# Optimization experiments

Hardware: AMD Instinct MI355X
Metric: run time of the kernel (lower is better)

Reference implementation:

```python
import jax, jax.numpy as jnp
import numpy as np

B, S, H = 16, 128, 768
L, K = 2, 4
NORM_ITEM = 0.5


def _xavier(key, shape):
    fan_in, fan_out = shape[-1], shape[-2]
    std = float(np.sqrt(2.0 / (fan_in + fan_out)))
    return jax.random.normal(key, shape, dtype=jnp.float32) * std


def setup_inputs() -> dict:
    key = jax.random.key(0)
    ks = jax.random.split(key, 13)
    sentences = jax.random.normal(ks[0], (B, S, H), dtype=jnp.float32)
    adj_matrix = jax.random.uniform(ks[1], (B, K, S, S), dtype=jnp.float32)
    return {
        "sentences": sentences,
        "adj_matrix": adj_matrix,
        # stacked per-(layer, dep_kind) parameters
        "W_in": _xavier(ks[2], (L, K, H, H)),
        "b_in": _xavier(ks[3], (L, K, H, 1)),
        "W_out": _xavier(ks[4], (L, K, H, H)),
        "b_out": _xavier(ks[5], (L, K, H, 1)),
        "Wg_in": _xavier(ks[6], (L, K, H, H)),
        "bg_in": _xavier(ks[7], (L, K, H, 1)),
        "Wg_out": _xavier(ks[8], (L, K, H, H)),
        "bg_out": _xavier(ks[9], (L, K, H, 1)),
        "W_loop": _xavier(ks[10], (L, H, H)),
    }


def reference(sentences, adj_matrix, W_in, b_in, W_out, b_out,
              Wg_in, bg_in, Wg_out, bg_out, W_loop):
    # sentences: [B,S,H], adj_matrix: [B,K,S,S]
    adj_in = adj_matrix                       # message along edges
    adj_out = jnp.swapaxes(adj_matrix, 2, 3)  # reversed edges
    h = jnp.swapaxes(sentences, 1, 2)         # [B,H,S]

    def conv(Wg, bg, W, b, adj, h):
        # Wg,W: [K,H,H]; bg,b: [K,H,1]; adj: [B,K,S,S]; h: [B,H,S]
        gate = jax.nn.sigmoid(jnp.einsum('khd,bds->bkhs', Wg, h) + bg[None])
        rel = NORM_ITEM * gate * (jnp.einsum('khd,bds->bkhs', W, h) + b[None])
        # bmm with adjacency, then sum over dep kinds
        return jnp.einsum('bkhs,bkst->bht', rel, adj)

    n_layers = W_in.shape[0]
    for l in range(n_layers):
        s = jnp.einsum('hd,bds->bhs', W_loop[l], h)  # self loop
        s = s + conv(Wg_in[l], bg_in[l], W_in[l], b_in[l], adj_in, h)
        s = s + conv(Wg_out[l], bg_out[l], W_out[l], b_out[l], adj_out, h)
        h = jax.nn.relu(s)
    return jnp.swapaxes(h, 1, 2)  # [B,S,H]
```

## Files before the change

kernel.cpp:

```cpp
#include <hip/hip_runtime.h>
#include <stdint.h>

#define B_ 16
#define S_ 128
#define H_ 768
#define K_ 4
#define L_ 2
#define T_ (B_*S_)

typedef __attribute__((ext_vector_type(4))) float f32x4;
typedef __attribute__((ext_vector_type(8))) short s16x8;
typedef __bf16 bf16x8 __attribute__((ext_vector_type(8)));
typedef unsigned short u16;

__device__ inline u16 f2bf(float f) {
    union { float f; uint32_t u; } v; v.f = f;
    uint32_t u = v.u;
    return (u16)((u + 0x7fffu + ((u >> 16) & 1u)) >> 16);
}

__device__ inline ushort4 f2bf4(float4 v) {
    ushort4 r; r.x = f2bf(v.x); r.y = f2bf(v.y); r.z = f2bf(v.z); r.w = f2bf(v.w);
    return r;
}

template <typename T>
__device__ inline auto mfma_impl(T a, T b, f32x4 c, int)
    -> decltype(__builtin_amdgcn_mfma_f32_16x16x32_bf16(a, b, c, 0, 0, 0)) {
    return __builtin_amdgcn_mfma_f32_16x16x32_bf16(a, b, c, 0, 0, 0);
}
template <typename T>
__device__ inline f32x4 mfma_impl(T a, T b, f32x4 c, long) {
    return __builtin_amdgcn_mfma_f32_16x16x32_bf16(
        __builtin_bit_cast(bf16x8, a), __builtin_bit_cast(bf16x8, b), c, 0, 0, 0);
}
__device__ inline f32x4 mfma16(s16x8 a, s16x8 b, f32x4 c) {
    return mfma_impl(a, b, c, 0);
}

__device__ inline void gload_lds16(const void* g, void* l) {
    __builtin_amdgcn_global_load_lds(
        (__attribute__((address_space(1))) void*)(g),
        (__attribute__((address_space(3))) void*)(l), 16, 0, 0);
}

__device__ inline void stage_tile(const char* gbase, int rowStrideBytes, u16* lds, int tid) {
    const int lane = tid & 63;
    const int w = tid >> 6;
    const int lr = lane >> 3;
    const int cb = (lane & 7) << 4;
    #pragma unroll
    for (int j = 0; j < 4; ++j) {
        const int seg = j * 4 + w;
        const int row = seg * 8 + lr;
        const int sb = cb ^ ((row & 7) << 4);
        gload_lds16(gbase + (size_t)row * rowStrideBytes + sb, lds + seg * 512);
    }
}

__device__ inline void stage64(const char* gbase, int rowStrideBytes, char* lds, int tid) {
    const int lane = tid & 63;
    const int w = tid >> 6;
    const int lr = lane >> 3;
    const int cb = (lane & 7) << 4;
    #pragma unroll
    for (int j = 0; j < 2; ++j) {
        const int seg = j * 4 + w;
        const int row = seg * 8 + lr;
        const int sb = cb ^ ((row & 7) << 4);
        gload_lds16(gbase + (size_t)row * rowStrideBytes + sb, lds + seg * 1024);
    }
}

__device__ inline s16x8 read_frag(const u16* lds, int row, int colByte) {
    const int bir = colByte ^ ((row & 7) << 4);
    return *(const s16x8*)((const char*)lds + row * 128 + bir);
}

__device__ inline s16x8 rf32s(const u16* lds, int row, int cb) {
    const int bir = cb ^ (((row >> 1) & 3) << 4);
    return *(const s16x8*)((const char*)lds + row * 64 + bir);
}

__global__ void prep_x(const float* __restrict__ sent, u16* __restrict__ X0) {
    const int i4 = blockIdx.x * blockDim.x + threadIdx.x;
    if (i4 < T_ * H_ / 4) ((ushort4*)X0)[i4] = f2bf4(((const float4*)sent)[i4]);
}

__global__ void prep_adj(const float* __restrict__ adj, u16* __restrict__ adjA) {
    const int idx = blockIdx.x * blockDim.x + threadIdx.x;
    const int s = idx & 127;
    const int t = (idx >> 7) & 127;
    const int b = (idx >> 14) & 15;
    const int p = idx >> 18;
    const int dir = p >> 2, k = p & 3;
    const float v = dir ? adj[(((size_t)b * K_ + k) * S_ + t) * S_ + s]
                        : adj[(((size_t)b * K_ + k) * S_ + s) * S_ + t];
    adjA[idx] = f2bf(v);
}

__global__ void pack_weights(const float* __restrict__ W_in,  const float* __restrict__ W_out,
                             const float* __restrict__ Wg_in, const float* __restrict__ Wg_out,
                             const float* __restrict__ W_loop, u16* __restrict__ Wpk) {
    __shared__ float slab[16][772];
    const int tid = threadIdx.x;
    const int bid = blockIdx.x;
    const int nT  = bid % 48;
    const int mat = (bid / 48) % 17;
    const int l   = bid / (48 * 17);

    const float* src;
    if (mat < 16) {
        const int p = mat >> 1, slot = mat & 1;
        const int dir = p >> 2, k = p & 3;
        const float* t = slot ? (dir ? Wg_out : Wg_in) : (dir ? W_out : W_in);
        src = t + ((size_t)l * K_ + k) * (H_ * H_);
    } else {
        src = W_loop + (size_t)l * (H_ * H_);
    }
    #pragma unroll
    for (int it = 0; it < 12; ++it) {
        const int idx = it * 256 + tid;
        const int row = idx / 192, c4 = idx % 192;
        *(float4*)&slab[row][c4 * 4] = ((const float4*)(src + (size_t)(nT * 16 + row) * H_))[c4];
    }
    __syncthreads();
    const int q = tid >> 6, lane = tid & 63;
    const int n = lane & 15, ks = lane >> 4;
    u16* outBase = Wpk + ((((size_t)l * 17 + mat) * 48 + nT) * 24) * 512;
    #pragma unroll
    for (int it = 0; it < 6; ++it) {
        const int kT = it * 4 + q;
        u16 tmp[8];
        #pragma unroll
        for (int u = 0; u < 8; ++u) tmp[u] = f2bf(slab[n][kT * 32 + ks * 8 + u]);
        s16x8 v;
        #pragma unroll
        for (int u = 0; u < 8; ++u) v[u] = (short)tmp[u];
        *(s16x8*)(outBase + (size_t)kT * 512 + lane * 8) = v;
    }
}

__global__ __launch_bounds__(256, 2)
void gemm1_kernel(const u16* __restrict__ Xb, const u16* __restrict__ Wpk,
                  const float* __restrict__ bg_in, const float* __restrict__ bg_out,
                  const float* __restrict__ b_in,  const float* __restrict__ b_out,
                  int layer,
                  u16* __restrict__ Rel2, float* __restrict__ SBuf) {
    __shared__ __align__(16) char smem[16384];

    const int tid = threadIdx.x;
    const int lane = tid & 63;
    const int w = tid >> 6;
    const int wm = w >> 1;
    const int wn = w & 1;
    const int l15 = lane & 15;
    const int hi16 = (lane >> 4) << 4;

    const int id = blockIdx.x;
    const int id2 = (id & 7) * 102 + (id >> 3);
    int p, y, m;
    if (id2 < 768) { p = id2 / 96; const int r = id2 % 96; y = r / 16; m = r % 16; }
    else           { const int q = id2 - 768; p = 8; y = q / 16; m = q % 16; }
    const int m0 = m * 128;

    const u16* pkL = Wpk + (size_t)layer * 17 * 589824;
    const int matR = (p < 8) ? p * 2     : 16;
    const int matG = (p < 8) ? p * 2 + 1 : 16;
    const int nbr  = (p < 8) ? y * 8     : y * 16;
    const int nbg  = (p < 8) ? y * 8     : y * 16 + 8;
    const u16* pR = pkL + ((size_t)matR * 48 + nbr + wn * 4) * (24 * 512) + lane * 8;
    const u16* pG = pkL + ((size_t)matG * 48 + nbg + wn * 4) * (24 * 512) + lane * 8;
    const char* gA = (const char*)Xb + (size_t)m0 * (H_ * 2);

    auto STAGE_A = [&](int kt, int c) {
        char* base = smem + c * 8192;
        #pragma unroll
        for (int j = 0; j < 2; ++j) {
            const int rr = (j * 4 + w) * 16 + (lane >> 2);
            const int cbl = (lane & 3) << 4;
            const int sc = cbl ^ (((rr >> 1) & 3) << 4);
            gload_lds16(gA + (size_t)rr * (H_ * 2) + kt * 64 + sc,
                        base + (j * 4 + w) * 1024);
        }
    };
    auto LOADB = [&](s16x8* dst, int kt) {
        #pragma unroll
        for (int j = 0; j < 4; ++j) {
            dst[j]     = *(const s16x8*)(pR + ((size_t)j * 24 + kt) * 512);
            dst[4 + j] = *(const s16x8*)(pG + ((size_t)j * 24 + kt) * 512);
        }
    };

    const f32x4 zf = {0.f, 0.f, 0.f, 0.f};
    f32x4 accr[4][4], accg[4][4];
    #pragma unroll
    for (int i = 0; i < 4; ++i)
        #pragma unroll
        for (int j = 0; j < 4; ++j) { accr[i][j] = zf; accg[i][j] = zf; }

    s16x8 bA[8], bB[8];

    STAGE_A(0, 0);
    __builtin_amdgcn_sched_barrier(0);
    LOADB(bA, 0);

    auto body = [&](int t, s16x8* cur, s16x8* nxt, bool pf) {
        asm volatile("s_waitcnt vmcnt(8)" ::: "memory");
        __builtin_amdgcn_s_barrier();
        const u16* lA = (const u16*)(smem + (t & 1) * 8192);
        s16x8 a[4];
        #pragma unroll
        for (int i = 0; i < 4; ++i)
            a[i] = rf32s(lA, wm * 64 + i * 16 + l15, hi16);
        if (pf) {
            STAGE_A(t + 1, (t + 1) & 1);
            __builtin_amdgcn_sched_barrier(0);
            LOADB(nxt, t + 1);
        }
        __builtin_amdgcn_s_setprio(1);
        #pragma unroll
        for (int i = 0; i < 4; ++i) {
            #pragma unroll
            for (int j = 0; j < 4; ++j) {
                accr[i][j] = mfma16(a[i], cur[j],     accr[i][j]);
                accg[i][j] = mfma16(a[i], cur[4 + j], accg[i][j]);
            }
        }
        __builtin_amdgcn_s_setprio(0);
    };

    for (int t = 0; t < 24; t += 2) {
        body(t,     bA, bB, true);
        body(t + 1, bB, bA, t + 1 < 23);
    }

    if (p < 8) {
        const int dir = p >> 2, k = p & 3;
        const float* bgp = (dir ? bg_out : bg_in) + ((size_t)layer * K_ + k) * H_;
        const float* brp = (dir ? b_out  : b_in ) + ((size_t)layer * K_ + k) * H_;
        #pragma unroll
        for (int j = 0; j < 4; ++j) {
            const int h = y * 128 + wn * 64 + j * 16 + l15;
            const float bgv = bgp[h];
            const float brv = brp[h];
            #pragma unroll
            for (int i = 0; i < 4; ++i) {
                const int s0 = wm * 64 + i * 16 + ((lane >> 4) << 2);
                u16 tmp[4];
                #pragma unroll
                for (int r = 0; r < 4; ++r) {
                    const float g = accg[i][j][r] + bgv;
                    const float v = accr[i][j][r] + brv;
                    tmp[r] = f2bf(0.5f * v / (1.f + __expf(-g)));
                }
                ushort4 pk; pk.x = tmp[0]; pk.y = tmp[1]; pk.z = tmp[2]; pk.w = tmp[3];
                *(ushort4*)(Rel2 + (((size_t)p * B_ + m) * H_ + h) * S_ + s0) = pk;
            }
        }
    } else {
        #pragma unroll
        for (int j = 0; j < 4; ++j) {
            const int h1 = y * 256 + wn * 64 + j * 16 + l15;
            const int h2 = h1 + 128;
            #pragma unroll
            for (int i = 0; i < 4; ++i) {
                const int tg = m0 + wm * 64 + i * 16 + ((lane >> 4) << 2);
                #pragma unroll
                for (int r = 0; r < 4; ++r) {
                    SBuf[(size_t)(tg + r) * H_ + h1] = accr[i][j][r];
                    SBuf[(size_t)(tg + r) * H_ + h2] = accg[i][j][r];
                }
            }
        }
    }
}

__global__ __launch_bounds__(256, 2)
void gemm2_kernel(const u16* __restrict__ adjA, const u16* __restrict__ Rel2,
                  const float* __restrict__ SBuf,
                  u16* __restrict__ Xn, float* __restrict__ Out, int lastLayer) {
    __shared__ __align__(16) char smem2[49152];

    const int tid = threadIdx.x;
    const int lane = tid & 63;
    const int w = tid >> 6;
    const int wm = w >> 1, wn = w & 1;
    const int l15 = lane & 15;
    const int hi16 = (lane >> 4) << 4;
    const int h0 = blockIdx.x * 64;
    const int b = blockIdx.y;

    auto STAGE = [&](int q, int c) {
        const int p = q >> 1, sc = q & 1;
        const char* Ab = (const char*)adjA + ((size_t)p * B_ + b) * (S_ * S_ * 2) + sc * 128;
        const char* Bb = (const char*)Rel2 + (((size_t)p * B_ + b) * H_ + h0) * (S_ * 2) + sc * 128;
        char* base = smem2 + c * 24576;
        stage_tile(Ab, S_ * 2, (u16*)base, tid);
        stage64(Bb, S_ * 2, base + 16384, tid);
    };

    const f32x4 zf = {0.f, 0.f, 0.f, 0.f};
    f32x4 acc[4][2];
    #pragma unroll
    for (int i = 0; i < 4; ++i)
        #pragma unroll
        for (int j = 0; j < 2; ++j) acc[i][j] = zf;

    STAGE(0, 0);
    __syncthreads();

    for (int q = 0; q < 16; ++q) {
        const int c = q & 1;
        if (q < 15) STAGE(q + 1, c ^ 1);
        const u16* lA = (const u16*)(smem2 + c * 24576);
        const u16* lB = (const u16*)(smem2 + c * 24576 + 16384);
        #pragma unroll
        for (int kq = 0; kq < 2; ++kq) {
            const int ck = kq * 64 + hi16;
            s16x8 a[4], bb[2];
            #pragma unroll
            for (int i = 0; i < 4; ++i)
                a[i] = read_frag(lA, wm * 64 + i * 16 + l15, ck);
            #pragma unroll
            for (int j = 0; j < 2; ++j)
                bb[j] = read_frag(lB, wn * 32 + j * 16 + l15, ck);
            #pragma unroll
            for (int i = 0; i < 4; ++i)
                #pragma unroll
                for (int j = 0; j < 2; ++j)
                    acc[i][j] = mfma16(a[i], bb[j], acc[i][j]);
        }
        __syncthreads();
    }

    #pragma unroll
    for (int i = 0; i < 4; ++i) {
        const int tl = wm * 64 + i * 16 + ((lane >> 4) << 2);
        #pragma unroll
        for (int j = 0; j < 2; ++j) {
            const int h = h0 + wn * 32 + j * 16 + l15;
            #pragma unroll
            for (int r = 0; r < 4; ++r) {
                const size_t t = (size_t)b * S_ + tl + r;
                float v = acc[i][j][r] + SBuf[t * H_ + h];
                v = fmaxf(v, 0.f);
                if (lastLayer) Out[t * H_ + h] = v;
                else           Xn[t * H_ + h] = f2bf(v);
            }
        }
    }
}

extern "C" void kernel_launch(void* const* d_in, const int* in_sizes, int n_in,
                              void* d_out, int out_size, void* d_ws, size_t ws_size,
                              hipStream_t stream) {
    const float* sent   = (const float*)d_in[0];
    const float* adj    = (const float*)d_in[1];
    const float* W_in   = (const float*)d_in[2];
    const float* b_in   = (const float*)d_in[3];
    const float* W_out  = (const float*)d_in[4];
    const float* b_out  = (const float*)d_in[5];
    const float* Wg_in  = (const float*)d_in[6];
    const float* bg_in  = (const float*)d_in[7];
    const float* Wg_out = (const float*)d_in[8];
    const float* bg_out = (const float*)d_in[9];
    const float* W_loop = (const float*)d_in[10];

    char* ws = (char*)d_ws;
    u16* Wpk    = (u16*)(ws);
    u16* adjA   = (u16*)(ws + 40108032);
    u16* X0     = (u16*)(ws + 44302336);
    u16* X1     = (u16*)(ws + 47448064);
    u16* Rel2   = (u16*)(ws + 50593792);
    float* SBuf = (float*)(ws + 75759616);

    prep_x<<<1536, 256, 0, stream>>>(sent, X0);
    prep_adj<<<8192, 256, 0, stream>>>(adj, adjA);
    pack_weights<<<L_ * 17 * 48, 256, 0, stream>>>(W_in, W_out, Wg_in, Wg_out, W_loop, Wpk);

    u16* Xc = X0;
    u16* Xn = X1;
    for (int l = 0; l < L_; ++l) {
        gemm1_kernel<<<816, 256, 0, stream>>>(Xc, Wpk, bg_in, bg_out, b_in, b_out,
                                              l, Rel2, SBuf);
        gemm2_kernel<<<dim3(12, 16), 256, 0, stream>>>(adjA, Rel2, SBuf, Xn,
                                                       (float*)d_out, l == L_ - 1);
        u16* t = Xc; Xc = Xn; Xn = t;
    }
}
```

Measured before the change: 186.6 us.

## Stage A tiles in 128-wide K chunks with 64KB LDS double buffer in gemm1

gemm1 now stages the activation tile into LDS in K-chunks of 128 (four MFMA sub-steps) instead of 32, using a 64KB double buffer with a new XOR swizzle. This cuts the number of block barriers from 24 to 6. B-fragment register loads are interleaved between the sub-steps. The cost is much higher LDS use per block, which may limit occupancy to about two blocks per CU.

```diff
diff --git a/kernel.cpp b/kernel.cpp
--- a/kernel.cpp
+++ b/kernel.cpp
@@ -77,9 +77,9 @@
     return *(const s16x8*)((const char*)lds + row * 128 + bir);
 }
 
-__device__ inline s16x8 rf32s(const u16* lds, int row, int cb) {
-    const int bir = cb ^ (((row >> 1) & 3) << 4);
-    return *(const s16x8*)((const char*)lds + row * 64 + bir);
+__device__ inline s16x8 rfA(const u16* lds, int row, int cb) {
+    const int bir = cb ^ ((row & 7) << 4);
+    return *(const s16x8*)((const char*)lds + row * 256 + bir);
 }
 
 __global__ void prep_x(const float* __restrict__ sent, u16* __restrict__ X0) {
@@ -147,7 +147,7 @@
                   const float* __restrict__ b_in,  const float* __restrict__ b_out,
                   int layer,
                   u16* __restrict__ Rel2, float* __restrict__ SBuf) {
-    __shared__ __align__(16) char smem[16384];
+    __shared__ __align__(16) char smem[65536];
 
     const int tid = threadIdx.x;
     const int lane = tid & 63;
@@ -155,7 +155,8 @@
     const int wm = w >> 1;
     const int wn = w & 1;
     const int l15 = lane & 15;
-    const int hi16 = (lane >> 4) << 4;
+    const int ks = lane >> 4;
+    const int hi16 = ks << 4;
 
     const int id = blockIdx.x;
     const int id2 = (id & 7) * 102 + (id >> 3);
@@ -173,15 +174,14 @@
     const u16* pG = pkL + ((size_t)matG * 48 + nbg + wn * 4) * (24 * 512) + lane * 8;
     const char* gA = (const char*)Xb + (size_t)m0 * (H_ * 2);
 
-    auto STAGE_A = [&](int kt, int c) {
-        char* base = smem + c * 8192;
-        #pragma unroll
-        for (int j = 0; j < 2; ++j) {
-            const int rr = (j * 4 + w) * 16 + (lane >> 2);
-            const int cbl = (lane & 3) << 4;
-            const int sc = cbl ^ (((rr >> 1) & 3) << 4);
-            gload_lds16(gA + (size_t)rr * (H_ * 2) + kt * 64 + sc,
-                        base + (j * 4 + w) * 1024);
+    auto STAGE_A = [&](int S, int c) {
+        char* base = smem + c * 32768;
+        #pragma unroll
+        for (int j = 0; j < 8; ++j) {
+            const int row = j * 16 + w * 4 + ks;
+            const int sc = (l15 << 4) ^ ((row & 7) << 4);
+            gload_lds16(gA + (size_t)row * (H_ * 2) + S * 256 + sc,
+                        base + j * 4096 + w * 1024);
         }
     };
     auto LOADB = [&](s16x8* dst, int kt) {
@@ -201,39 +201,44 @@
 
     s16x8 bA[8], bB[8];
 
+    #define DO_SUB(LA, KTL, BUF)                                               \
+        {                                                                      \
+            s16x8 a[4];                                                        \
+            _Pragma("unroll") for (int i = 0; i < 4; ++i)                      \
+                a[i] = rfA(LA, wm * 64 + i * 16 + l15, (KTL) * 64 + hi16);     \
+            __builtin_amdgcn_s_setprio(1);                                     \
+            _Pragma("unroll") for (int i = 0; i < 4; ++i) {                    \
+                _Pragma("unroll") for (int j = 0; j < 4; ++j) {                \
+                    accr[i][j] = mfma16(a[i], BUF[j],     accr[i][j]);         \
+                    accg[i][j] = mfma16(a[i], BUF[4 + j], accg[i][j]);         \
+                }                                                              \
+            }                                                                  \
+            __builtin_amdgcn_s_setprio(0);                                     \
+        }
+
     STAGE_A(0, 0);
+    LOADB(bA, 0);
+    asm volatile("s_waitcnt vmcnt(0)" ::: "memory");
+    __builtin_amdgcn_s_barrier();
     __builtin_amdgcn_sched_barrier(0);
-    LOADB(bA, 0);
-
-    auto body = [&](int t, s16x8* cur, s16x8* nxt, bool pf) {
+
+    for (int S = 0; S < 6; ++S) {
+        const u16* lA = (const u16*)(smem + (S & 1) * 32768);
+        const int k0 = S * 4;
+        LOADB(bB, k0 + 1);
+        if (S < 5) STAGE_A(S + 1, (S & 1) ^ 1);
+        DO_SUB(lA, 0, bA)
+        LOADB(bA, k0 + 2);
+        DO_SUB(lA, 1, bB)
+        LOADB(bB, k0 + 3);
+        DO_SUB(lA, 2, bA)
+        if (S < 5) LOADB(bA, k0 + 4);
+        DO_SUB(lA, 3, bB)
         asm volatile("s_waitcnt vmcnt(8)" ::: "memory");
         __builtin_amdgcn_s_barrier();
-        const u16* lA = (const u16*)(smem + (t & 1) * 8192);
-        s16x8 a[4];
-        #pragma unroll
-        for (int i = 0; i < 4; ++i)
-            a[i] = rf32s(lA, wm * 64 + i * 16 + l15, hi16);
-        if (pf) {
-            STAGE_A(t + 1, (t + 1) & 1);
-            __builtin_amdgcn_sched_barrier(0);
-            LOADB(nxt, t + 1);
-        }
-        __builtin_amdgcn_s_setprio(1);
-        #pragma unroll
-        for (int i = 0; i < 4; ++i) {
-            #pragma unroll
-            for (int j = 0; j < 4; ++j) {
-                accr[i][j] = mfma16(a[i], cur[j],     accr[i][j]);
-                accg[i][j] = mfma16(a[i], cur[4 + j], accg[i][j]);
-            }
-        }
-        __builtin_amdgcn_s_setprio(0);
-    };
-
-    for (int t = 0; t < 24; t += 2) {
-        body(t,     bA, bB, true);
-        body(t + 1, bB, bA, t + 1 < 23);
-    }
+        __builtin_amdgcn_sched_barrier(0);
+    }
+    #undef DO_SUB
 
     if (p < 8) {
         const int dir = p >> 2, k = p & 3;
@@ -246,7 +251,7 @@
             const float brv = brp[h];
             #pragma unroll
             for (int i = 0; i < 4; ++i) {
-                const int s0 = wm * 64 + i * 16 + ((lane >> 4) << 2);
+                const int s0 = wm * 64 + i * 16 + ks * 4;
                 u16 tmp[4];
                 #pragma unroll
                 for (int r = 0; r < 4; ++r) {
@@ -265,7 +270,7 @@
             const int h2 = h1 + 128;
             #pragma unroll
             for (int i = 0; i < 4; ++i) {
-                const int tg = m0 + wm * 64 + i * 16 + ((lane >> 4) << 2);
+                const int tg = m0 + wm * 64 + i * 16 + ks * 4;
                 #pragma unroll
                 for (int r = 0; r < 4; ++r) {
                     SBuf[(size_t)(tg + r) * H_ + h1] = accr[i][j][r];
```

After: 174.7 us. 6.4% less time.

## Switch gemm1 to 32x32x16 MFMA with smaller tiles and split gate/value roles

Applied to the files above, without the earlier changes.

Repacks weights for the 32x32x16 bf16 MFMA layout and rewrites gemm1 so each block computes a 128x64 tile. Warps specialise by role: some compute the gate projection and others the value projection, and the sigmoid is exchanged through LDS in the epilogue. The grid is doubled and occupancy raised to 4 blocks per CU, with a reworked double-buffered pipeline. The aim is better MFMA efficiency and latency hiding, at the cost of an extra LDS exchange and barrier in the epilogue and lower per-block operand reuse.

```diff
diff --git a/kernel.cpp b/kernel.cpp
--- a/kernel.cpp
+++ b/kernel.cpp
@@ -9,6 +9,7 @@
 #define T_ (B_*S_)
 
 typedef __attribute__((ext_vector_type(4))) float f32x4;
+typedef __attribute__((ext_vector_type(16))) float f32x16;
 typedef __attribute__((ext_vector_type(8))) short s16x8;
 typedef __bf16 bf16x8 __attribute__((ext_vector_type(8)));
 typedef unsigned short u16;
@@ -25,17 +26,31 @@
 }
 
 template <typename T>
-__device__ inline auto mfma_impl(T a, T b, f32x4 c, int)
+__device__ inline auto mfma16_impl(T a, T b, f32x4 c, int)
     -> decltype(__builtin_amdgcn_mfma_f32_16x16x32_bf16(a, b, c, 0, 0, 0)) {
     return __builtin_amdgcn_mfma_f32_16x16x32_bf16(a, b, c, 0, 0, 0);
 }
 template <typename T>
-__device__ inline f32x4 mfma_impl(T a, T b, f32x4 c, long) {
+__device__ inline f32x4 mfma16_impl(T a, T b, f32x4 c, long) {
     return __builtin_amdgcn_mfma_f32_16x16x32_bf16(
         __builtin_bit_cast(bf16x8, a), __builtin_bit_cast(bf16x8, b), c, 0, 0, 0);
 }
 __device__ inline f32x4 mfma16(s16x8 a, s16x8 b, f32x4 c) {
-    return mfma_impl(a, b, c, 0);
+    return mfma16_impl(a, b, c, 0);
+}
+
+template <typename T>
+__device__ inline auto mfma32_impl(T a, T b, f32x16 c, int)
+    -> decltype(__builtin_amdgcn_mfma_f32_32x32x16_bf16(a, b, c, 0, 0, 0)) {
+    return __builtin_amdgcn_mfma_f32_32x32x16_bf16(a, b, c, 0, 0, 0);
+}
+template <typename T>
+__device__ inline f32x16 mfma32_impl(T a, T b, f32x16 c, long) {
+    return __builtin_amdgcn_mfma_f32_32x32x16_bf16(
+        __builtin_bit_cast(bf16x8, a), __builtin_bit_cast(bf16x8, b), c, 0, 0, 0);
+}
+__device__ inline f32x16 mfma32(s16x8 a, s16x8 b, f32x16 c) {
+    return mfma32_impl(a, b, c, 0);
 }
 
 __device__ inline void gload_lds16(const void* g, void* l) {
@@ -75,11 +90,6 @@
 __device__ inline s16x8 read_frag(const u16* lds, int row, int colByte) {
     const int bir = colByte ^ ((row & 7) << 4);
     return *(const s16x8*)((const char*)lds + row * 128 + bir);
-}
-
-__device__ inline s16x8 rf32s(const u16* lds, int row, int cb) {
-    const int bir = cb ^ (((row >> 1) & 3) << 4);
-    return *(const s16x8*)((const char*)lds + row * 64 + bir);
 }
 
 __global__ void prep_x(const float* __restrict__ sent, u16* __restrict__ X0) {
@@ -99,15 +109,15 @@
     adjA[idx] = f2bf(v);
 }
 
-__global__ void pack_weights(const float* __restrict__ W_in,  const float* __restrict__ W_out,
-                             const float* __restrict__ Wg_in, const float* __restrict__ Wg_out,
-                             const float* __restrict__ W_loop, u16* __restrict__ Wpk) {
-    __shared__ float slab[16][772];
+__global__ void pack_weights32(const float* __restrict__ W_in,  const float* __restrict__ W_out,
+                               const float* __restrict__ Wg_in, const float* __restrict__ Wg_out,
+                               const float* __restrict__ W_loop, u16* __restrict__ Wpk) {
+    __shared__ u16 slab[32][776];
     const int tid = threadIdx.x;
     const int bid = blockIdx.x;
-    const int nT  = bid % 48;
-    const int mat = (bid / 48) % 17;
-    const int l   = bid / (48 * 17);
+    const int nT  = bid % 24;
+    const int mat = (bid / 24) % 17;
+    const int l   = bid / (24 * 17);
 
     const float* src;
     if (mat < 16) {
@@ -119,157 +129,186 @@
         src = W_loop + (size_t)l * (H_ * H_);
     }
     #pragma unroll
-    for (int it = 0; it < 12; ++it) {
+    for (int it = 0; it < 24; ++it) {
         const int idx = it * 256 + tid;
         const int row = idx / 192, c4 = idx % 192;
-        *(float4*)&slab[row][c4 * 4] = ((const float4*)(src + (size_t)(nT * 16 + row) * H_))[c4];
+        float4 v = ((const float4*)(src + (size_t)(nT * 32 + row) * H_))[c4];
+        slab[row][c4 * 4 + 0] = f2bf(v.x);
+        slab[row][c4 * 4 + 1] = f2bf(v.y);
+        slab[row][c4 * 4 + 2] = f2bf(v.z);
+        slab[row][c4 * 4 + 3] = f2bf(v.w);
     }
     __syncthreads();
     const int q = tid >> 6, lane = tid & 63;
-    const int n = lane & 15, ks = lane >> 4;
-    u16* outBase = Wpk + ((((size_t)l * 17 + mat) * 48 + nT) * 24) * 512;
-    #pragma unroll
-    for (int it = 0; it < 6; ++it) {
+    const int row = lane & 31, kg = lane >> 5;
+    u16* outBase = Wpk + (((size_t)(l * 17 + mat) * 24 + nT) * 48) * 512;
+    #pragma unroll
+    for (int it = 0; it < 12; ++it) {
         const int kT = it * 4 + q;
-        u16 tmp[8];
-        #pragma unroll
-        for (int u = 0; u < 8; ++u) tmp[u] = f2bf(slab[n][kT * 32 + ks * 8 + u]);
-        s16x8 v;
-        #pragma unroll
-        for (int u = 0; u < 8; ++u) v[u] = (short)tmp[u];
+        s16x8 v = *(const s16x8*)&slab[row][kT * 16 + kg * 8];
         *(s16x8*)(outBase + (size_t)kT * 512 + lane * 8) = v;
     }
 }
 
-__global__ __launch_bounds__(256, 2)
+__global__ __launch_bounds__(256, 4)
 void gemm1_kernel(const u16* __restrict__ Xb, const u16* __restrict__ Wpk,
                   const float* __restrict__ bg_in, const float* __restrict__ bg_out,
                   const float* __restrict__ b_in,  const float* __restrict__ b_out,
                   int layer,
                   u16* __restrict__ Rel2, float* __restrict__ SBuf) {
-    __shared__ __align__(16) char smem[16384];
+    __shared__ __align__(16) char smem[32768];
 
     const int tid = threadIdx.x;
     const int lane = tid & 63;
     const int w = tid >> 6;
     const int wm = w >> 1;
-    const int wn = w & 1;
-    const int l15 = lane & 15;
-    const int hi16 = (lane >> 4) << 4;
+    const int role = w & 1;
+    const int l31 = lane & 31;
+    const int kg = lane >> 5;
 
     const int id = blockIdx.x;
-    const int id2 = (id & 7) * 102 + (id >> 3);
+    const int task = (id & 7) * 204 + (id >> 3);
     int p, y, m;
-    if (id2 < 768) { p = id2 / 96; const int r = id2 % 96; y = r / 16; m = r % 16; }
-    else           { const int q = id2 - 768; p = 8; y = q / 16; m = q % 16; }
+    if (task < 1536) { p = task / 192; const int r = task % 192; y = r / 16; m = r % 16; }
+    else             { const int q2 = task - 1536; p = 8; y = q2 / 16; m = q2 % 16; }
     const int m0 = m * 128;
 
-    const u16* pkL = Wpk + (size_t)layer * 17 * 589824;
-    const int matR = (p < 8) ? p * 2     : 16;
-    const int matG = (p < 8) ? p * 2 + 1 : 16;
-    const int nbr  = (p < 8) ? y * 8     : y * 16;
-    const int nbg  = (p < 8) ? y * 8     : y * 16 + 8;
-    const u16* pR = pkL + ((size_t)matR * 48 + nbr + wn * 4) * (24 * 512) + lane * 8;
-    const u16* pG = pkL + ((size_t)matG * 48 + nbg + wn * 4) * (24 * 512) + lane * 8;
+    int mat, nT0;
+    if (p < 8) { mat = p * 2 + role; nT0 = y * 2; }
+    else       { mat = 16;           nT0 = y * 4 + role * 2; }
+    const u16* pB = Wpk + (((size_t)(layer * 17 + mat) * 24 + nT0) * 48) * 512 + lane * 8;
     const char* gA = (const char*)Xb + (size_t)m0 * (H_ * 2);
 
-    auto STAGE_A = [&](int kt, int c) {
+    auto STAGE_A = [&](int t, int c) {
         char* base = smem + c * 8192;
         #pragma unroll
         for (int j = 0; j < 2; ++j) {
-            const int rr = (j * 4 + w) * 16 + (lane >> 2);
-            const int cbl = (lane & 3) << 4;
-            const int sc = cbl ^ (((rr >> 1) & 3) << 4);
-            gload_lds16(gA + (size_t)rr * (H_ * 2) + kt * 64 + sc,
-                        base + (j * 4 + w) * 1024);
+            const int srow = j * 64 + w * 16 + (lane >> 2);
+            const int sc = (lane & 3) ^ ((srow >> 1) & 3);
+            gload_lds16(gA + (size_t)srow * (H_ * 2) + t * 64 + sc * 16,
+                        base + (j * 256 + w * 64) * 16);
         }
     };
-    auto LOADB = [&](s16x8* dst, int kt) {
-        #pragma unroll
-        for (int j = 0; j < 4; ++j) {
-            dst[j]     = *(const s16x8*)(pR + ((size_t)j * 24 + kt) * 512);
-            dst[4 + j] = *(const s16x8*)(pG + ((size_t)j * 24 + kt) * 512);
-        }
+    auto LOADB = [&](s16x8* dst, int t) {
+        #pragma unroll
+        for (int j = 0; j < 2; ++j)
+            #pragma unroll
+            for (int kq = 0; kq < 2; ++kq)
+                dst[j * 2 + kq] = *(const s16x8*)(pB + ((size_t)j * 48 + 2 * t + kq) * 512);
     };
 
-    const f32x4 zf = {0.f, 0.f, 0.f, 0.f};
-    f32x4 accr[4][4], accg[4][4];
-    #pragma unroll
-    for (int i = 0; i < 4; ++i)
-        #pragma unroll
-        for (int j = 0; j < 4; ++j) { accr[i][j] = zf; accg[i][j] = zf; }
-
-    s16x8 bA[8], bB[8];
+    f32x16 acc[2][2];
+    #pragma unroll
+    for (int q = 0; q < 2; ++q)
+        #pragma unroll
+        for (int j = 0; j < 2; ++j) acc[q][j] = (f32x16)(0.0f);
+
+    s16x8 bA[4], bB[4];
 
     STAGE_A(0, 0);
+    LOADB(bA, 0);
+    asm volatile("s_waitcnt vmcnt(0)" ::: "memory");
+    __builtin_amdgcn_s_barrier();
     __builtin_amdgcn_sched_barrier(0);
-    LOADB(bA, 0);
-
-    auto body = [&](int t, s16x8* cur, s16x8* nxt, bool pf) {
-        asm volatile("s_waitcnt vmcnt(8)" ::: "memory");
+
+    auto body = [&](int t, s16x8* cur, s16x8* nxt) {
+        const int c = t & 1;
+        if (t < 23) { STAGE_A(t + 1, c ^ 1); LOADB(nxt, t + 1); }
+        __builtin_amdgcn_sched_barrier(0);
+        const u16* lA = (const u16*)(smem + c * 8192);
+        s16x8 a[2][2];
+        #pragma unroll
+        for (int q = 0; q < 2; ++q)
+            #pragma unroll
+            for (int kq = 0; kq < 2; ++kq) {
+                const int row = wm * 64 + q * 32 + l31;
+                const int o16 = (kq * 2 + kg) ^ ((row >> 1) & 3);
+                a[q][kq] = *(const s16x8*)((const char*)lA + row * 64 + o16 * 16);
+            }
+        asm volatile("s_waitcnt vmcnt(6)" ::: "memory");
+        __builtin_amdgcn_sched_barrier(0);
+        __builtin_amdgcn_s_setprio(1);
+        #pragma unroll
+        for (int q = 0; q < 2; ++q)
+            #pragma unroll
+            for (int j = 0; j < 2; ++j)
+                #pragma unroll
+                for (int kq = 0; kq < 2; ++kq)
+                    acc[q][j] = mfma32(a[q][kq], cur[j * 2 + kq], acc[q][j]);
+        __builtin_amdgcn_s_setprio(0);
+        asm volatile("s_waitcnt vmcnt(4)" ::: "memory");
         __builtin_amdgcn_s_barrier();
-        const u16* lA = (const u16*)(smem + (t & 1) * 8192);
-        s16x8 a[4];
-        #pragma unroll
-        for (int i = 0; i < 4; ++i)
-            a[i] = rf32s(lA, wm * 64 + i * 16 + l15, hi16);
-        if (pf) {
-            STAGE_A(t + 1, (t + 1) & 1);
-            __builtin_amdgcn_sched_barrier(0);
-            LOADB(nxt, t + 1);
-        }
-        __builtin_amdgcn_s_setprio(1);
-        #pragma unroll
-        for (int i = 0; i < 4; ++i) {
-            #pragma unroll
-            for (int j = 0; j < 4; ++j) {
-                accr[i][j] = mfma16(a[i], cur[j],     accr[i][j]);
-                accg[i][j] = mfma16(a[i], cur[4 + j], accg[i][j]);
+        __builtin_amdgcn_sched_barrier(0);
+    };
+
+    for (int t = 0; t < 24; t += 2) {
+        body(t, bA, bB);
+        body(t + 1, bB, bA);
+    }
+
+    if (p < 8) {
+        const int dir = p >> 2, kk = p & 3;
+        float* sig = (float*)smem;
+        if (role == 1) {
+            const float* bgp = (dir ? bg_out : bg_in) + ((size_t)layer * K_ + kk) * H_;
+            #pragma unroll
+            for (int q = 0; q < 2; ++q) {
+                #pragma unroll
+                for (int j = 0; j < 2; ++j) {
+                    const int col = j * 32 + l31;
+                    const float bgv = bgp[y * 64 + col];
+                    #pragma unroll
+                    for (int g = 0; g < 4; ++g) {
+                        const int tok0 = wm * 64 + q * 32 + g * 8 + kg * 4;
+                        f32x4 sv;
+                        #pragma unroll
+                        for (int rr = 0; rr < 4; ++rr) {
+                            const float gv = acc[q][j][g * 4 + rr] + bgv;
+                            sv[rr] = 1.f / (1.f + __expf(-gv));
+                        }
+                        *(f32x4*)((char*)sig + ((col * 512 + tok0 * 4) ^ ((col & 7) << 4))) = sv;
+                    }
+                }
             }
         }
-        __builtin_amdgcn_s_setprio(0);
-    };
-
-    for (int t = 0; t < 24; t += 2) {
-        body(t,     bA, bB, true);
-        body(t + 1, bB, bA, t + 1 < 23);
-    }
-
-    if (p < 8) {
-        const int dir = p >> 2, k = p & 3;
-        const float* bgp = (dir ? bg_out : bg_in) + ((size_t)layer * K_ + k) * H_;
-        const float* brp = (dir ? b_out  : b_in ) + ((size_t)layer * K_ + k) * H_;
-        #pragma unroll
-        for (int j = 0; j < 4; ++j) {
-            const int h = y * 128 + wn * 64 + j * 16 + l15;
-            const float bgv = bgp[h];
-            const float brv = brp[h];
-            #pragma unroll
-            for (int i = 0; i < 4; ++i) {
-                const int s0 = wm * 64 + i * 16 + ((lane >> 4) << 2);
-                u16 tmp[4];
+        __syncthreads();
+        if (role == 0) {
+            const float* brp = (dir ? b_out : b_in) + ((size_t)layer * K_ + kk) * H_;
+            #pragma unroll
+            for (int q = 0; q < 2; ++q) {
                 #pragma unroll
-                for (int r = 0; r < 4; ++r) {
-                    const float g = accg[i][j][r] + bgv;
-                    const float v = accr[i][j][r] + brv;
-                    tmp[r] = f2bf(0.5f * v / (1.f + __expf(-g)));
+                for (int j = 0; j < 2; ++j) {
+                    const int col = j * 32 + l31;
+                    const int h = y * 64 + col;
+                    const float brv = brp[h];
+                    u16* dst = Rel2 + (((size_t)p * B_ + m) * H_ + h) * S_;
+                    #pragma unroll
+                    for (int g = 0; g < 4; ++g) {
+                        const int tok0 = wm * 64 + q * 32 + g * 8 + kg * 4;
+                        f32x4 sv = *(const f32x4*)((const char*)sig +
+                                   ((col * 512 + tok0 * 4) ^ ((col & 7) << 4)));
+                        ushort4 pk;
+                        pk.x = f2bf(0.5f * (acc[q][j][g * 4 + 0] + brv) * sv[0]);
+                        pk.y = f2bf(0.5f * (acc[q][j][g * 4 + 1] + brv) * sv[1]);
+                        pk.z = f2bf(0.5f * (acc[q][j][g * 4 + 2] + brv) * sv[2]);
+                        pk.w = f2bf(0.5f * (acc[q][j][g * 4 + 3] + brv) * sv[3]);
+                        *(ushort4*)(dst + tok0) = pk;
+                    }
                 }
-                ushort4 pk; pk.x = tmp[0]; pk.y = tmp[1]; pk.z = tmp[2]; pk.w = tmp[3];
-                *(ushort4*)(Rel2 + (((size_t)p * B_ + m) * H_ + h) * S_ + s0) = pk;
             }
         }
     } else {
         #pragma unroll
-        for (int j = 0; j < 4; ++j) {
-            const int h1 = y * 256 + wn * 64 + j * 16 + l15;
-            const int h2 = h1 + 128;
-            #pragma unroll
-            for (int i = 0; i < 4; ++i) {
-                const int tg = m0 + wm * 64 + i * 16 + ((lane >> 4) << 2);
+        for (int q = 0; q < 2; ++q) {
+            #pragma unroll
+            for (int j = 0; j < 2; ++j) {
+                const int h = y * 128 + role * 64 + j * 32 + l31;
                 #pragma unroll
-                for (int r = 0; r < 4; ++r) {
-                    SBuf[(size_t)(tg + r) * H_ + h1] = accr[i][j][r];
-                    SBuf[(size_t)(tg + r) * H_ + h2] = accg[i][j][r];
+                for (int g = 0; g < 4; ++g) {
+                    const int tok0 = m0 + wm * 64 + q * 32 + g * 8 + kg * 4;
+                    #pragma unroll
+                    for (int rr = 0; rr < 4; ++rr)
+                        SBuf[(size_t)(tok0 + rr) * H_ + h] = acc[q][j][g * 4 + rr];
                 }
             }
         }
@@ -377,13 +416,13 @@
 
     prep_x<<<1536, 256, 0, stream>>>(sent, X0);
     prep_adj<<<8192, 256, 0, stream>>>(adj, adjA);
-    pack_weights<<<L_ * 17 * 48, 256, 0, stream>>>(W_in, W_out, Wg_in, Wg_out, W_loop, Wpk);
+    pack_weights32<<<L_ * 17 * 24, 256, 0, stream>>>(W_in, W_out, Wg_in, Wg_out, W_loop, Wpk);
 
     u16* Xc = X0;
     u16* Xn = X1;
     for (int l = 0; l < L_; ++l) {
-        gemm1_kernel<<<816, 256, 0, stream>>>(Xc, Wpk, bg_in, bg_out, b_in, b_out,
-                                              l, Rel2, SBuf);
+        gemm1_kernel<<<1632, 256, 0, stream>>>(Xc, Wpk, bg_in, bg_out, b_in, b_out,
+                                               l, Rel2, SBuf);
         gemm2_kernel<<<dim3(12, 16), 256, 0, stream>>>(adjA, Rel2, SBuf, Xn,
                                                        (float*)d_out, l == L_ - 1);
         u16* t = Xc; Xc = Xn; Xn = t;
```

Measured after the change: 204.5 us. +9.6%, slower.
